# Performance work log

Measured on AMD Instinct MI355X. Metric: run time of the kernel, lower is better.

Reference implementation:

```python
import jax, jax.numpy as jnp
import numpy as np
from math import factorial

# ---- configuration (from init_kwargs irreps strings) ----
IRR1 = [(128, 0, 1), (128, 1, -1), (128, 2, 1)]   # (mul, l, parity)
IRR2 = [(1, 0, 1), (1, 1, -1), (1, 2, 1)]
IRRO = [(128, 0, 1), (128, 1, -1), (128, 2, 1)]
BATCH = 32768

# ---- real-basis Wigner 3j (e3nn convention: unit Frobenius norm) ----

def _cg_coeff(j1, m1, j2, m2, j3, m3):
    f = factorial
    vmin = int(max(-j1 + j2 + m3, -j1 + m1, 0))
    vmax = int(min(j2 + j3 + m1, j3 - j1 + j2, j3 + m3))
    C = ((2 * j3 + 1) * f(j3 + j1 - j2) * f(j3 - j1 + j2) * f(j1 + j2 - j3)
         * f(j3 + m3) * f(j3 - m3)
         / (f(j1 + j2 + j3 + 1) * f(j1 - m1) * f(j1 + m1) * f(j2 - m2) * f(j2 + m2))) ** 0.5
    S = 0.0
    for v in range(vmin, vmax + 1):
        S += (-1.0) ** (v + j2 + m2) * f(j2 + j3 + m1 - v) * f(j1 - m1 + v) / (
            f(v) * f(j3 - j1 + j2 - v) * f(j3 + m3 - v) * f(v + j1 - j2 - m3))
    return C * S


def _su2_cg(j1, j2, j3):
    m = np.zeros((2 * j1 + 1, 2 * j2 + 1, 2 * j3 + 1))
    for m1 in range(-j1, j1 + 1):
        for m2 in range(-j2, j2 + 1):
            m3 = m1 + m2
            if abs(m3) <= j3:
                m[j1 + m1, j2 + m2, j3 + m3] = _cg_coeff(j1, m1, j2, m2, j3, m3)
    return m


def _q(l):  # change of basis real -> complex spherical harmonics
    q = np.zeros((2 * l + 1, 2 * l + 1), dtype=np.complex128)
    for m in range(-l, 0):
        q[l + m, l + abs(m)] = 1 / np.sqrt(2)
        q[l + m, l - abs(m)] = -1j / np.sqrt(2)
    q[l, l] = 1.0
    for m in range(1, l + 1):
        q[l + m, l + abs(m)] = (-1) ** m / np.sqrt(2)
        q[l + m, l - abs(m)] = 1j * (-1) ** m / np.sqrt(2)
    return (-1j) ** l * q


def wigner_3j(l1, l2, l3):
    C = _su2_cg(l1, l2, l3).astype(np.complex128)
    C = np.einsum('ij,kl,mn,ikn->jlm', _q(l1), _q(l2), np.conj(_q(l3).T), C)
    C = np.real(C)
    return (C / np.linalg.norm(C)).astype(np.float32)


# ---- instructions: all allowed uvw paths (same triple loop as the torch module) ----

def _build_instructions():
    instr = []
    for i1, (m1, l1, p1) in enumerate(IRR1):
        for i2, (m2, l2, p2) in enumerate(IRR2):
            for io, (mo, lo, po) in enumerate(IRRO):
                if abs(l1 - l2) <= lo <= l1 + l2 and p1 * p2 == po:
                    instr.append((i1, i2, io))
    # e3nn defaults: irrep_normalization='component', path_normalization='element'
    elem = {}
    for (i1, i2, io) in instr:
        elem[io] = elem.get(io, 0) + IRR1[i1][0] * IRR2[i2][0]
    pathw = [((2 * IRRO[io][1] + 1) / elem[io]) ** 0.5 for (i1, i2, io) in instr]
    return instr, pathw

INSTR, PATHW = _build_instructions()
OFF1 = np.cumsum([0] + [m * (2 * l + 1) for m, l, _ in IRR1]).tolist()
OFF2 = np.cumsum([0] + [m * (2 * l + 1) for m, l, _ in IRR2]).tolist()
OFFO = np.cumsum([0] + [m * (2 * l + 1) for m, l, _ in IRRO]).tolist()
W3J = {(i1, i2, io): jnp.asarray(wigner_3j(IRR1[i1][1], IRR2[i2][1], IRRO[io][1]))
       for (i1, i2, io) in INSTR}


def setup_inputs() -> dict:
    key = jax.random.key(0)
    k1, k2, k3, k4 = jax.random.split(key, 4)
    n = len(INSTR)  # 11
    return {
        'x1': jax.random.normal(k1, (BATCH, OFF1[-1]), jnp.float32),
        'x2': jax.random.normal(k2, (BATCH, OFF2[-1]), jnp.float32),
        'w1': jax.random.normal(k3, (n, IRR1[0][0], IRRO[0][0]), jnp.float32),
        'w2': jax.random.normal(k4, (n, IRR2[0][0], IRRO[0][0]), jnp.float32),
    }


def reference(x1, x2, w1, w2):
    # fused per-path CG contraction: weight W[u,v,w] = w1[u,w] * w2[v,w]
    B = x1.shape[0]
    acc = [None] * len(IRRO)
    for idx, (i1, i2, io) in enumerate(INSTR):
        m1, l1, _ = IRR1[i1]
        m2, l2, _ = IRR2[i2]
        mo, lo, _ = IRRO[io]
        a = x1[:, OFF1[i1]:OFF1[i1 + 1]].reshape(B, m1, 2 * l1 + 1)  # (B,u,i)
        b = x2[:, OFF2[i2]:OFF2[i2 + 1]].reshape(B, m2, 2 * l2 + 1)  # (B,v,j)
        C = W3J[(i1, i2, io)] * PATHW[idx]                            # (i,j,k)
        o = jnp.einsum('uw,vw,ijk,bui,bvj->bwk', w1[idx], w2[idx], C, a, b,
                       optimize='optimal').reshape(B, mo * (2 * lo + 1))
        acc[io] = o if acc[io] is None else acc[io] + o
    return jnp.concatenate(acc, axis=1)
```

## Files before the change

kernel.cpp:

```cpp
#include <hip/hip_runtime.h>

typedef float f32x4v __attribute__((ext_vector_type(4)));
typedef short s16x8  __attribute__((ext_vector_type(8)));

#define MT 32

constexpr int cI1[11]   = {0,0,0,1,1,1,1,2,2,2,2};
constexpr int cI2[11]   = {0,1,2,0,1,1,2,0,1,2,2};
constexpr int cIO[11]   = {0,1,2,1,0,2,1,2,1,0,2};
constexpr int cSOFF[11] = {0,1,4,9,18,21,36,45,70,85,90};
constexpr int cOFF1[3]  = {0,128,512};
constexpr int cOFF2[3]  = {0,1,4};

__device__ __forceinline__ unsigned short f2bf(float f){
  unsigned int u = __float_as_uint(f);
  u = u + 0x7fffu + ((u>>16)&1u);
  return (unsigned short)(u>>16);
}

__device__ __forceinline__ float ffact(int n){ float r=1.f; for(int i=2;i<=n;++i) r*=(float)i; return r; }

__device__ float cg1f(int j1,int m1,int j2,int m2,int j3,int m3){
  int vmin = -j1+j2+m3; int t=-j1+m1; if(t>vmin)vmin=t; if(vmin<0)vmin=0;
  int vmax = j2+j3+m1; t=j3-j1+j2; if(t<vmax)vmax=t; t=j3+m3; if(t<vmax)vmax=t;
  float C = sqrtf((2.f*j3+1.f)*ffact(j3+j1-j2)*ffact(j3-j1+j2)*ffact(j1+j2-j3)
                 *ffact(j3+m3)*ffact(j3-m3)
                 /(ffact(j1+j2+j3+1)*ffact(j1-m1)*ffact(j1+m1)*ffact(j2-m2)*ffact(j2+m2)));
  float S=0.f;
  for(int v=vmin;v<=vmax;++v){
    float sg = ((v+j2+m2)&1)? -1.f:1.f;
    S += sg*ffact(j2+j3+m1-v)*ffact(j1-m1+v)
        /(ffact(v)*ffact(j3-j1+j2-v)*ffact(j3+m3-v)*ffact(v+j1-j2-m3));
  }
  return C*S;
}

__global__ void prep_cg(float* __restrict__ wsC){
  __shared__ float s_cg[125];
  __shared__ float s_qr[3][25], s_qi[3][25];
  __shared__ float s_out[125];
  __shared__ float s_inv;
  const int idx = blockIdx.x;
  const int l1=cI1[idx], l2=cI2[idx], l3=cIO[idx];
  const int n1=2*l1+1, n2=2*l2+1, n3=2*l3+1;
  const int tid = threadIdx.x;
  if (tid < 125) s_cg[tid] = 0.f;
  __syncthreads();
  if (tid < 75){
    const int mat=tid/25, e=tid%25, a=e/5, b=e%5;
    const int l = (mat==0)?l1:((mat==1)?l2:l3);
    const int n = 2*l+1;
    float r=0.f, im=0.f;
    if (a<n && b<n){
      const int m = a - l;
      const float s2 = 0.70710678118654752440f;
      if (m < 0){
        if (b == l-m) r = s2;
        else if (b == a) im = -s2;
      } else if (m == 0){
        if (b == a) r = 1.f;
      } else {
        const float sg = (m&1)? -1.f:1.f;
        if (b == a) r = sg*s2;
        else if (b == l-m) im = sg*s2;
      }
      const int ph = l & 3;
      if (ph == 1){ float t=r; r=im; im=-t; }
      else if (ph == 2){ r=-r; im=-im; }
      else if (ph == 3){ float t=r; r=-im; im=t; }
    }
    s_qr[mat][e] = r; s_qi[mat][e] = im;
  }
  if (tid < n1*n2){
    const int m1 = tid / n2 - l1;
    const int m2 = tid % n2 - l2;
    const int m3 = m1 + m2;
    if (m3 >= -l3 && m3 <= l3)
      s_cg[(l1+m1)*25 + (l2+m2)*5 + (l3+m3)] = cg1f(l1,m1,l2,m2,l3,m3);
  }
  __syncthreads();
  const int nElem = n1*n2*n3;
  if (tid < nElem){
    const int j = tid/(n2*n3);
    const int L = (tid/n3) % n2;
    const int m = tid % n3;
    float acc = 0.f;
    for (int i=0;i<n1;i++){
      const float ar=s_qr[0][i*5+j], ai=s_qi[0][i*5+j];
      for (int k=0;k<n2;k++){
        const float br=s_qr[1][k*5+L], bi=s_qi[1][k*5+L];
        const float pr=ar*br-ai*bi, pi=ar*bi+ai*br;
        for (int n=0;n<n3;n++){
          const float c=s_cg[i*25+k*5+n];
          acc += c*(pr*s_qr[2][n*5+m] + pi*s_qi[2][n*5+m]);
        }
      }
    }
    s_out[tid] = acc;
  }
  __syncthreads();
  if (tid == 0){
    float nrm = 0.f;
    for (int t=0;t<nElem;t++) nrm += s_out[t]*s_out[t];
    s_inv = rsqrtf(nrm);
  }
  __syncthreads();
  if (tid < 125){
    const int j=tid/25, L=(tid/5)%5, m=tid%5;
    float v = 0.f;
    if (j<n1 && L<n2 && m<n3) v = s_out[(j*n2+L)*n3+m] * s_inv;
    wsC[idx*125 + tid] = v;
  }
}

__global__ void prep_w(const float* __restrict__ w1, const float* __restrict__ w2,
                       unsigned char* __restrict__ wsB){
  int gid = blockIdx.x*256 + threadIdx.x;
  if (gid >= 11*8*4*64) return;
  int lane = gid & 63;
  int g = gid >> 6;
  int kst = g & 3, nt = (g>>2)&7, idx = g>>5;
  int io = cIO[idx];
  float pw = (io==0)?0.051031036307982884f:((io==1)?0.07654655446197431f:0.09882117688026186f);
  int u0 = kst*32 + ((lane>>4)&3)*8;
  int w  = nt*16 + (lane&15);
  float w2v = w2[idx*128 + w] * pw;
  s16x8 p;
  #pragma unroll
  for (int e=0;e<8;e++){
    float v = w1[idx*16384 + (u0+e)*128 + w] * w2v;
    p[e] = (short)f2bf(v);
  }
  *(s16x8*)(wsB + (size_t)g*1024 + (size_t)lane*16) = p;
}

template<int IDX, int NK>
__device__ __forceinline__ void do_idx(f32x4v (&acc)[NK][2],
    const float* __restrict__ x1, const unsigned char* __restrict__ wsB,
    unsigned char* lds, const float* s_lds, int brow0, int tid){
  constexpr int I1 = cI1[IDX];
  constexpr int NI = 2*I1+1;
  const int lane = tid & 63, wave = tid >> 6;
  const int mtile = wave >> 2, ng0 = (wave & 3)*2;
  s16x8 bfr[2][4];
  #pragma unroll
  for(int nt=0;nt<2;nt++)
    #pragma unroll
    for(int kst=0;kst<4;kst++)
      bfr[nt][kst] = *(const s16x8*)(wsB + (size_t)(((IDX*8 + ng0+nt)*4 + kst)*64 + lane)*16);
  const int tb = tid >> 4, tu0 = (tid & 15)*8;
  const float* xrow = x1 + (size_t)(brow0+tb)*1152 + cOFF1[I1] + tu0*NI;
  const int row = mtile*16 + (lane&15);
  const int rsw = (row&7)<<4;
  const int hi  = (lane>>4)&3;
  f32x4v xv[2*NI];
  #pragma unroll
  for(int f=0;f<2*NI;f++) xv[f] = ((const f32x4v*)xrow)[f];
  #pragma unroll
  for(int kc0=0;kc0<NK;kc0+=3){
    __syncthreads();
    #pragma unroll
    for(int kk=0;kk<3;kk++) if(kc0+kk<NK){
      const int k=kc0+kk;
      float sv[NI];
      #pragma unroll
      for(int i=0;i<NI;i++) sv[i]=s_lds[tb*116 + cSOFF[IDX] + i*NK + k];
      s16x8 tp;
      #pragma unroll
      for(int u=0;u<8;u++){
        float tvv=0.0f;
        #pragma unroll
        for(int i=0;i<NI;i++){ const int n=u*NI+i; tvv += sv[i]*xv[n>>2][n&3]; }
        tp[u]=(short)f2bf(tvv);
      }
      *(s16x8*)(lds + kk*8192 + tb*256 + ((tu0*2) ^ ((tb&7)<<4))) = tp;
    }
    __syncthreads();
    #pragma unroll
    for(int kk=0;kk<3;kk++) if(kc0+kk<NK){
      #pragma unroll
      for(int kst=0;kst<4;kst++){
        s16x8 af = *(const s16x8*)(lds + kk*8192 + row*256 + ((kst*64 + hi*16) ^ rsw));
        #pragma unroll
        for(int nt=0;nt<2;nt++)
          acc[kc0+kk][nt] = __builtin_amdgcn_mfma_f32_16x16x32_bf16(af, bfr[nt][kst], acc[kc0+kk][nt], 0,0,0);
      }
    }
  }
}

template<int OO, int NK>
__device__ __forceinline__ void store_group(f32x4v (&acc)[NK][2], float* __restrict__ out, int brow0, int tid){
  const int lane=tid&63, wave=tid>>6;
  const int mtile=wave>>2, ng0=(wave&3)*2;
  const int r0 = brow0 + mtile*16 + ((lane>>4)&3)*4;
  #pragma unroll
  for(int nt=0;nt<2;nt++){
    const int w = (ng0+nt)*16 + (lane&15);
    #pragma unroll
    for(int k=0;k<NK;k++){
      #pragma unroll
      for(int rr=0;rr<4;rr++)
        out[(size_t)(r0+rr)*1152 + OO + w*NK + k] = acc[k][nt][rr];
    }
  }
}

__global__ __launch_bounds__(512) void tp_main(
    const float* __restrict__ x1, const float* __restrict__ x2,
    const float* __restrict__ wsC, const unsigned char* __restrict__ wsB,
    float* __restrict__ out){
  __shared__ __attribute__((aligned(16))) unsigned char lds[24576 + 32*116*4];
  float* s_lds = (float*)(lds + 24576);
  const int tid = threadIdx.x;
  const int brow0 = blockIdx.x * MT;
  if (tid < 352){
    const int b = tid & 31, idx = tid >> 5;
    const int i1=cI1[idx], i2=cI2[idx], io=cIO[idx];
    const int ni=2*i1+1, nj=2*i2+1, nk=2*io+1;
    const float* x2r = x2 + (size_t)(brow0+b)*9 + cOFF2[i2];
    const float* C = wsC + idx*125;
    float xv[5];
    for(int j=0;j<nj;j++) xv[j]=x2r[j];
    for(int i=0;i<ni;i++)
      for(int k=0;k<nk;k++){
        float s=0.f;
        for(int j=0;j<nj;j++) s += C[i*25+j*5+k]*xv[j];
        s_lds[b*116 + cSOFF[idx] + i*nk + k] = s;
      }
  }
  {
    f32x4v acc[1][2] = {};
    do_idx<0,1>(acc,x1,wsB,lds,s_lds,brow0,tid);
    do_idx<4,1>(acc,x1,wsB,lds,s_lds,brow0,tid);
    do_idx<9,1>(acc,x1,wsB,lds,s_lds,brow0,tid);
    store_group<0,1>(acc,out,brow0,tid);
  }
  {
    f32x4v acc[3][2] = {};
    do_idx<1,3>(acc,x1,wsB,lds,s_lds,brow0,tid);
    do_idx<3,3>(acc,x1,wsB,lds,s_lds,brow0,tid);
    do_idx<6,3>(acc,x1,wsB,lds,s_lds,brow0,tid);
    do_idx<8,3>(acc,x1,wsB,lds,s_lds,brow0,tid);
    store_group<128,3>(acc,out,brow0,tid);
  }
  {
    f32x4v acc[5][2] = {};
    do_idx<2,5>(acc,x1,wsB,lds,s_lds,brow0,tid);
    do_idx<5,5>(acc,x1,wsB,lds,s_lds,brow0,tid);
    do_idx<7,5>(acc,x1,wsB,lds,s_lds,brow0,tid);
    do_idx<10,5>(acc,x1,wsB,lds,s_lds,brow0,tid);
    store_group<512,5>(acc,out,brow0,tid);
  }
}

extern "C" void kernel_launch(void* const* d_in, const int* in_sizes, int n_in,
                              void* d_out, int out_size, void* d_ws, size_t ws_size,
                              hipStream_t stream) {
  const float* x1 = (const float*)d_in[0];
  const float* x2 = (const float*)d_in[1];
  const float* w1 = (const float*)d_in[2];
  const float* w2 = (const float*)d_in[3];
  float* out = (float*)d_out;
  float* wsC = (float*)d_ws;
  unsigned char* wsB = (unsigned char*)d_ws + 8192;
  prep_cg<<<11, 128, 0, stream>>>(wsC);
  prep_w<<<88, 256, 0, stream>>>(w1, w2, wsB);
  tp_main<<<32768/MT, 512, 0, stream>>>(x1, x2, wsC, wsB, out);
}
```

Baseline: 408.9 us.

## Double-buffer LDS tiles and software-pipeline T build with MFMA consumption

Replaces the per-path loop (sync, build bf16 T tile in LDS, sync, MFMA) with a hand-unrolled software pipeline over two LDS buffers. The build of the next chunk and the prefetch of the next x1 rows and B fragments overlap the MFMAs on the current buffer, and one barrier per stage replaces two. LDS use doubles to about 61 KB per block, which may reduce how many blocks fit per CU, and register pressure rises from the prefetched xv and bfr.

```diff
diff --git a/kernel.cpp b/kernel.cpp
--- a/kernel.cpp
+++ b/kernel.cpp
@@ -134,57 +134,63 @@
   *(s16x8*)(wsB + (size_t)g*1024 + (size_t)lane*16) = p;
 }
 
-template<int IDX, int NK>
-__device__ __forceinline__ void do_idx(f32x4v (&acc)[NK][2],
-    const float* __restrict__ x1, const unsigned char* __restrict__ wsB,
-    unsigned char* lds, const float* s_lds, int brow0, int tid){
-  constexpr int I1 = cI1[IDX];
-  constexpr int NI = 2*I1+1;
-  const int lane = tid & 63, wave = tid >> 6;
-  const int mtile = wave >> 2, ng0 = (wave & 3)*2;
-  s16x8 bfr[2][4];
+
+template<int IDX>
+__device__ __forceinline__ void xv_load(f32x4v (&xv)[10], const float* __restrict__ x1, int brow0, int tid){
+  constexpr int NI = 2*cI1[IDX]+1;
+  const int tb = tid>>4, tu0 = (tid&15)*8;
+  const float* xrow = x1 + (size_t)(brow0+tb)*1152 + cOFF1[cI1[IDX]] + tu0*NI;
+  #pragma unroll
+  for(int f=0; f<2*NI; f++) xv[f] = ((const f32x4v*)xrow)[f];
+}
+
+template<int IDX>
+__device__ __forceinline__ void bfr_load(s16x8 (&bfr)[2][4], const unsigned char* __restrict__ wsB, int tid){
+  const int lane=tid&63, wave=tid>>6, ng0=(wave&3)*2;
   #pragma unroll
   for(int nt=0;nt<2;nt++)
     #pragma unroll
     for(int kst=0;kst<4;kst++)
-      bfr[nt][kst] = *(const s16x8*)(wsB + (size_t)(((IDX*8 + ng0+nt)*4 + kst)*64 + lane)*16);
-  const int tb = tid >> 4, tu0 = (tid & 15)*8;
-  const float* xrow = x1 + (size_t)(brow0+tb)*1152 + cOFF1[I1] + tu0*NI;
+      bfr[nt][kst] = *(const s16x8*)(wsB + (size_t)(((IDX*8+ng0+nt)*4+kst)*64+lane)*16);
+}
+
+template<int IDX, int NK, int KB, int NKC>
+__device__ __forceinline__ void t_build(const f32x4v (&xv)[10], unsigned char* buf,
+                                        const float* s_lds, int tid){
+  constexpr int NI = 2*cI1[IDX]+1;
+  const int tb = tid>>4, tu0=(tid&15)*8;
+  #pragma unroll
+  for(int kk=0;kk<NKC;kk++){
+    const int k = KB+kk;
+    float sv[NI];
+    #pragma unroll
+    for(int i=0;i<NI;i++) sv[i] = s_lds[tb*116 + cSOFF[IDX] + i*NK + k];
+    s16x8 tp;
+    #pragma unroll
+    for(int u=0;u<8;u++){
+      float t=0.f;
+      #pragma unroll
+      for(int i=0;i<NI;i++){ const int n=u*NI+i; t += sv[i]*xv[n>>2][n&3]; }
+      tp[u]=(short)f2bf(t);
+    }
+    *(s16x8*)(buf + kk*8192 + tb*256 + ((tu0*2) ^ ((tb&7)<<4))) = tp;
+  }
+}
+
+template<int NACC, int KB, int NKC>
+__device__ __forceinline__ void mfma_cons(f32x4v (&acc)[NACC][2], const s16x8 (&bfr)[2][4],
+                                          const unsigned char* buf, int tid){
+  const int lane=tid&63, wave=tid>>6, mtile=wave>>2;
   const int row = mtile*16 + (lane&15);
-  const int rsw = (row&7)<<4;
-  const int hi  = (lane>>4)&3;
-  f32x4v xv[2*NI];
-  #pragma unroll
-  for(int f=0;f<2*NI;f++) xv[f] = ((const f32x4v*)xrow)[f];
-  #pragma unroll
-  for(int kc0=0;kc0<NK;kc0+=3){
-    __syncthreads();
-    #pragma unroll
-    for(int kk=0;kk<3;kk++) if(kc0+kk<NK){
-      const int k=kc0+kk;
-      float sv[NI];
+  const int rsw = (row&7)<<4, hi=(lane>>4)&3;
+  #pragma unroll
+  for(int kk=0;kk<NKC;kk++){
+    #pragma unroll
+    for(int kst=0;kst<4;kst++){
+      s16x8 af = *(const s16x8*)(buf + kk*8192 + row*256 + ((kst*64+hi*16)^rsw));
       #pragma unroll
-      for(int i=0;i<NI;i++) sv[i]=s_lds[tb*116 + cSOFF[IDX] + i*NK + k];
-      s16x8 tp;
-      #pragma unroll
-      for(int u=0;u<8;u++){
-        float tvv=0.0f;
-        #pragma unroll
-        for(int i=0;i<NI;i++){ const int n=u*NI+i; tvv += sv[i]*xv[n>>2][n&3]; }
-        tp[u]=(short)f2bf(tvv);
-      }
-      *(s16x8*)(lds + kk*8192 + tb*256 + ((tu0*2) ^ ((tb&7)<<4))) = tp;
-    }
-    __syncthreads();
-    #pragma unroll
-    for(int kk=0;kk<3;kk++) if(kc0+kk<NK){
-      #pragma unroll
-      for(int kst=0;kst<4;kst++){
-        s16x8 af = *(const s16x8*)(lds + kk*8192 + row*256 + ((kst*64 + hi*16) ^ rsw));
-        #pragma unroll
-        for(int nt=0;nt<2;nt++)
-          acc[kc0+kk][nt] = __builtin_amdgcn_mfma_f32_16x16x32_bf16(af, bfr[nt][kst], acc[kc0+kk][nt], 0,0,0);
-      }
+      for(int nt=0;nt<2;nt++)
+        acc[KB+kk][nt] = __builtin_amdgcn_mfma_f32_16x16x32_bf16(af, bfr[nt][kst], acc[KB+kk][nt],0,0,0);
     }
   }
 }
@@ -210,47 +216,112 @@
     const float* __restrict__ x1, const float* __restrict__ x2,
     const float* __restrict__ wsC, const unsigned char* __restrict__ wsB,
     float* __restrict__ out){
-  __shared__ __attribute__((aligned(16))) unsigned char lds[24576 + 32*116*4];
-  float* s_lds = (float*)(lds + 24576);
+  __shared__ __attribute__((aligned(16))) unsigned char lds[49152 + 32*116*4];
+  unsigned char* buf0 = lds;
+  unsigned char* buf1 = lds + 24576;
+  float* s_lds = (float*)(lds + 49152);
   const int tid = threadIdx.x;
   const int brow0 = blockIdx.x * MT;
+
   if (tid < 352){
     const int b = tid & 31, idx = tid >> 5;
     const int i1=cI1[idx], i2=cI2[idx], io=cIO[idx];
     const int ni=2*i1+1, nj=2*i2+1, nk=2*io+1;
     const float* x2r = x2 + (size_t)(brow0+b)*9 + cOFF2[i2];
     const float* C = wsC + idx*125;
-    float xv[5];
-    for(int j=0;j<nj;j++) xv[j]=x2r[j];
+    float xv2[5];
+    for(int j=0;j<nj;j++) xv2[j]=x2r[j];
     for(int i=0;i<ni;i++)
       for(int k=0;k<nk;k++){
         float s=0.f;
-        for(int j=0;j<nj;j++) s += C[i*25+j*5+k]*xv[j];
+        for(int j=0;j<nj;j++) s += C[i*25+j*5+k]*xv2[j];
         s_lds[b*116 + cSOFF[idx] + i*nk + k] = s;
       }
   }
+
+  f32x4v xv[10];
+  s16x8 bfr[2][4];
+
+  xv_load<0>(xv, x1, brow0, tid);
+  bfr_load<0>(bfr, wsB, tid);
+  __syncthreads();
+  t_build<0,1,0,1>(xv, buf0, s_lds, tid);
+  xv_load<4>(xv, x1, brow0, tid);
+  __syncthreads();
+
   {
-    f32x4v acc[1][2] = {};
-    do_idx<0,1>(acc,x1,wsB,lds,s_lds,brow0,tid);
-    do_idx<4,1>(acc,x1,wsB,lds,s_lds,brow0,tid);
-    do_idx<9,1>(acc,x1,wsB,lds,s_lds,brow0,tid);
-    store_group<0,1>(acc,out,brow0,tid);
+    f32x4v accA[1][2] = {};
+    mfma_cons<1,0,1>(accA, bfr, buf0, tid);
+    t_build<4,1,0,1>(xv, buf1, s_lds, tid);
+    xv_load<9>(xv, x1, brow0, tid);
+    bfr_load<4>(bfr, wsB, tid);
+    __syncthreads();
+    mfma_cons<1,0,1>(accA, bfr, buf1, tid);
+    t_build<9,1,0,1>(xv, buf0, s_lds, tid);
+    xv_load<1>(xv, x1, brow0, tid);
+    bfr_load<9>(bfr, wsB, tid);
+    __syncthreads();
+    mfma_cons<1,0,1>(accA, bfr, buf0, tid);
+    t_build<1,3,0,3>(xv, buf1, s_lds, tid);
+    xv_load<3>(xv, x1, brow0, tid);
+    bfr_load<1>(bfr, wsB, tid);
+    store_group<0,1>(accA, out, brow0, tid);
+    __syncthreads();
   }
   {
-    f32x4v acc[3][2] = {};
-    do_idx<1,3>(acc,x1,wsB,lds,s_lds,brow0,tid);
-    do_idx<3,3>(acc,x1,wsB,lds,s_lds,brow0,tid);
-    do_idx<6,3>(acc,x1,wsB,lds,s_lds,brow0,tid);
-    do_idx<8,3>(acc,x1,wsB,lds,s_lds,brow0,tid);
-    store_group<128,3>(acc,out,brow0,tid);
+    f32x4v accB[3][2] = {};
+    mfma_cons<3,0,3>(accB, bfr, buf1, tid);
+    t_build<3,3,0,3>(xv, buf0, s_lds, tid);
+    xv_load<6>(xv, x1, brow0, tid);
+    bfr_load<3>(bfr, wsB, tid);
+    __syncthreads();
+    mfma_cons<3,0,3>(accB, bfr, buf0, tid);
+    t_build<6,3,0,3>(xv, buf1, s_lds, tid);
+    xv_load<8>(xv, x1, brow0, tid);
+    bfr_load<6>(bfr, wsB, tid);
+    __syncthreads();
+    mfma_cons<3,0,3>(accB, bfr, buf1, tid);
+    t_build<8,3,0,3>(xv, buf0, s_lds, tid);
+    xv_load<2>(xv, x1, brow0, tid);
+    bfr_load<8>(bfr, wsB, tid);
+    __syncthreads();
+    mfma_cons<3,0,3>(accB, bfr, buf0, tid);
+    t_build<2,5,0,3>(xv, buf1, s_lds, tid);
+    bfr_load<2>(bfr, wsB, tid);
+    store_group<128,3>(accB, out, brow0, tid);
+    __syncthreads();
   }
   {
-    f32x4v acc[5][2] = {};
-    do_idx<2,5>(acc,x1,wsB,lds,s_lds,brow0,tid);
-    do_idx<5,5>(acc,x1,wsB,lds,s_lds,brow0,tid);
-    do_idx<7,5>(acc,x1,wsB,lds,s_lds,brow0,tid);
-    do_idx<10,5>(acc,x1,wsB,lds,s_lds,brow0,tid);
-    store_group<512,5>(acc,out,brow0,tid);
+    f32x4v accC[5][2] = {};
+    mfma_cons<5,0,3>(accC, bfr, buf1, tid);
+    t_build<2,5,3,2>(xv, buf0, s_lds, tid);
+    xv_load<5>(xv, x1, brow0, tid);
+    __syncthreads();
+    mfma_cons<5,3,2>(accC, bfr, buf0, tid);
+    t_build<5,5,0,3>(xv, buf1, s_lds, tid);
+    bfr_load<5>(bfr, wsB, tid);
+    __syncthreads();
+    mfma_cons<5,0,3>(accC, bfr, buf1, tid);
+    t_build<5,5,3,2>(xv, buf0, s_lds, tid);
+    xv_load<7>(xv, x1, brow0, tid);
+    __syncthreads();
+    mfma_cons<5,3,2>(accC, bfr, buf0, tid);
+    t_build<7,5,0,3>(xv, buf1, s_lds, tid);
+    bfr_load<7>(bfr, wsB, tid);
+    __syncthreads();
+    mfma_cons<5,0,3>(accC, bfr, buf1, tid);
+    t_build<7,5,3,2>(xv, buf0, s_lds, tid);
+    xv_load<10>(xv, x1, brow0, tid);
+    __syncthreads();
+    mfma_cons<5,3,2>(accC, bfr, buf0, tid);
+    t_build<10,5,0,3>(xv, buf1, s_lds, tid);
+    bfr_load<10>(bfr, wsB, tid);
+    __syncthreads();
+    mfma_cons<5,0,3>(accC, bfr, buf1, tid);
+    t_build<10,5,3,2>(xv, buf0, s_lds, tid);
+    __syncthreads();
+    mfma_cons<5,3,2>(accC, bfr, buf0, tid);
+    store_group<512,5>(accC, out, brow0, tid);
   }
 }
 
```

Measured after the change: 389.7 us. -4.7%, faster.

## Reorder contraction to GEMM per x1 component, then scale by CG-x2 terms

Applied to the files above, without the earlier changes.

Each x1 irrep block is now converted to bf16 and staged in LDS once, split by component. The kernel then runs one MFMA GEMM per component i, then applies the per-row s[b,i,k] coefficients to the fp32 results and adds them into accumulators held for all three outputs. Before, it built a separate combined activation tile for every (path, k) pair. This cuts the repeated x1 global loads, the fp32 combine work, the bf16 conversions and the barriers per path. In exchange, all three accumulator sets stay live at once, which raises register pressure, and the staging step uses strided scalar global reads.

```diff
diff --git a/kernel.cpp b/kernel.cpp
--- a/kernel.cpp
+++ b/kernel.cpp
@@ -134,56 +134,78 @@
   *(s16x8*)(wsB + (size_t)g*1024 + (size_t)lane*16) = p;
 }
 
-template<int IDX, int NK>
-__device__ __forceinline__ void do_idx(f32x4v (&acc)[NK][2],
-    const float* __restrict__ x1, const unsigned char* __restrict__ wsB,
-    unsigned char* lds, const float* s_lds, int brow0, int tid){
-  constexpr int I1 = cI1[IDX];
+
+template<int I1>
+__device__ __forceinline__ void stage_x(const float* __restrict__ x1, unsigned char* xt,
+                                        int brow0, int tid){
   constexpr int NI = 2*I1+1;
-  const int lane = tid & 63, wave = tid >> 6;
-  const int mtile = wave >> 2, ng0 = (wave & 3)*2;
+  const int b = tid>>4, oct = tid&15;
+  const float* src = x1 + (size_t)(brow0+b)*1152 + cOFF1[I1];
+  const int dsw = (oct*16) ^ ((b&7)<<4);
+  if constexpr (I1==0){
+    f32x4v v0 = *(const f32x4v*)(src + oct*8);
+    f32x4v v1 = *(const f32x4v*)(src + oct*8 + 4);
+    s16x8 p;
+    #pragma unroll
+    for(int e=0;e<4;e++){ p[e]=(short)f2bf(v0[e]); p[4+e]=(short)f2bf(v1[e]); }
+    *(s16x8*)(xt + b*256 + dsw) = p;
+  } else if constexpr (I1==1){
+    s16x8 p0, p1, p2;
+    #pragma unroll
+    for(int e=0;e<8;e++){
+      const float* q = src + (oct*8+e)*3;
+      p0[e]=(short)f2bf(q[0]); p1[e]=(short)f2bf(q[1]); p2[e]=(short)f2bf(q[2]);
+    }
+    *(s16x8*)(xt            + b*256 + dsw) = p0;
+    *(s16x8*)(xt +   8192   + b*256 + dsw) = p1;
+    *(s16x8*)(xt + 2*8192   + b*256 + dsw) = p2;
+  } else {
+    s16x8 p0, p1, p2, p3, p4;
+    #pragma unroll
+    for(int e=0;e<8;e++){
+      const float* q = src + (oct*8+e)*5;
+      p0[e]=(short)f2bf(q[0]); p1[e]=(short)f2bf(q[1]); p2[e]=(short)f2bf(q[2]);
+      p3[e]=(short)f2bf(q[3]); p4[e]=(short)f2bf(q[4]);
+    }
+    *(s16x8*)(xt            + b*256 + dsw) = p0;
+    *(s16x8*)(xt +   8192   + b*256 + dsw) = p1;
+    *(s16x8*)(xt + 2*8192   + b*256 + dsw) = p2;
+    *(s16x8*)(xt + 3*8192   + b*256 + dsw) = p3;
+    *(s16x8*)(xt + 4*8192   + b*256 + dsw) = p4;
+  }
+}
+
+template<int P, int NKT>
+__device__ __forceinline__ void path_compute(f32x4v (&acc)[NKT][2],
+    const unsigned char* xt, const float* s_lds, const unsigned char* __restrict__ wsB, int tid){
+  constexpr int NI = 2*cI1[P]+1;
+  const int lane=tid&63, wave=tid>>6, mtile=wave>>2, ng0=(wave&3)*2;
   s16x8 bfr[2][4];
   #pragma unroll
   for(int nt=0;nt<2;nt++)
     #pragma unroll
     for(int kst=0;kst<4;kst++)
-      bfr[nt][kst] = *(const s16x8*)(wsB + (size_t)(((IDX*8 + ng0+nt)*4 + kst)*64 + lane)*16);
-  const int tb = tid >> 4, tu0 = (tid & 15)*8;
-  const float* xrow = x1 + (size_t)(brow0+tb)*1152 + cOFF1[I1] + tu0*NI;
-  const int row = mtile*16 + (lane&15);
-  const int rsw = (row&7)<<4;
-  const int hi  = (lane>>4)&3;
-  f32x4v xv[2*NI];
-  #pragma unroll
-  for(int f=0;f<2*NI;f++) xv[f] = ((const f32x4v*)xrow)[f];
-  #pragma unroll
-  for(int kc0=0;kc0<NK;kc0+=3){
-    __syncthreads();
-    #pragma unroll
-    for(int kk=0;kk<3;kk++) if(kc0+kk<NK){
-      const int k=kc0+kk;
-      float sv[NI];
+      bfr[nt][kst] = *(const s16x8*)(wsB + (size_t)(((P*8+ng0+nt)*4+kst)*64+lane)*16);
+  const int arow = mtile*16 + (lane&15);
+  const int rsw  = (arow&7)<<4;
+  const int hi   = lane>>4;
+  const int sbase = (mtile*16 + hi*4)*116 + cSOFF[P];
+  #pragma unroll
+  for(int i=0;i<NI;i++){
+    f32x4v Y0 = {0.f,0.f,0.f,0.f}, Y1 = {0.f,0.f,0.f,0.f};
+    #pragma unroll
+    for(int kst=0;kst<4;kst++){
+      s16x8 af = *(const s16x8*)(xt + i*8192 + arow*256 + ((kst*64 + hi*16) ^ rsw));
+      Y0 = __builtin_amdgcn_mfma_f32_16x16x32_bf16(af, bfr[0][kst], Y0, 0,0,0);
+      Y1 = __builtin_amdgcn_mfma_f32_16x16x32_bf16(af, bfr[1][kst], Y1, 0,0,0);
+    }
+    #pragma unroll
+    for(int r=0;r<4;r++){
       #pragma unroll
-      for(int i=0;i<NI;i++) sv[i]=s_lds[tb*116 + cSOFF[IDX] + i*NK + k];
-      s16x8 tp;
-      #pragma unroll
-      for(int u=0;u<8;u++){
-        float tvv=0.0f;
-        #pragma unroll
-        for(int i=0;i<NI;i++){ const int n=u*NI+i; tvv += sv[i]*xv[n>>2][n&3]; }
-        tp[u]=(short)f2bf(tvv);
-      }
-      *(s16x8*)(lds + kk*8192 + tb*256 + ((tu0*2) ^ ((tb&7)<<4))) = tp;
-    }
-    __syncthreads();
-    #pragma unroll
-    for(int kk=0;kk<3;kk++) if(kc0+kk<NK){
-      #pragma unroll
-      for(int kst=0;kst<4;kst++){
-        s16x8 af = *(const s16x8*)(lds + kk*8192 + row*256 + ((kst*64 + hi*16) ^ rsw));
-        #pragma unroll
-        for(int nt=0;nt<2;nt++)
-          acc[kc0+kk][nt] = __builtin_amdgcn_mfma_f32_16x16x32_bf16(af, bfr[nt][kst], acc[kc0+kk][nt], 0,0,0);
+      for(int k=0;k<NKT;k++){
+        const float sv = s_lds[sbase + r*116 + i*NKT + k];
+        acc[k][0][r] += sv * Y0[r];
+        acc[k][1][r] += sv * Y1[r];
       }
     }
   }
@@ -210,48 +232,55 @@
     const float* __restrict__ x1, const float* __restrict__ x2,
     const float* __restrict__ wsC, const unsigned char* __restrict__ wsB,
     float* __restrict__ out){
-  __shared__ __attribute__((aligned(16))) unsigned char lds[24576 + 32*116*4];
-  float* s_lds = (float*)(lds + 24576);
+  __shared__ __attribute__((aligned(16))) unsigned char lds[40960 + 32*116*4];
+  unsigned char* xt = lds;
+  float* s_lds = (float*)(lds + 40960);
   const int tid = threadIdx.x;
   const int brow0 = blockIdx.x * MT;
+
   if (tid < 352){
     const int b = tid & 31, idx = tid >> 5;
     const int i1=cI1[idx], i2=cI2[idx], io=cIO[idx];
     const int ni=2*i1+1, nj=2*i2+1, nk=2*io+1;
     const float* x2r = x2 + (size_t)(brow0+b)*9 + cOFF2[i2];
     const float* C = wsC + idx*125;
-    float xv[5];
-    for(int j=0;j<nj;j++) xv[j]=x2r[j];
+    float xv2[5];
+    for(int j=0;j<nj;j++) xv2[j]=x2r[j];
     for(int i=0;i<ni;i++)
       for(int k=0;k<nk;k++){
         float s=0.f;
-        for(int j=0;j<nj;j++) s += C[i*25+j*5+k]*xv[j];
+        for(int j=0;j<nj;j++) s += C[i*25+j*5+k]*xv2[j];
         s_lds[b*116 + cSOFF[idx] + i*nk + k] = s;
       }
   }
-  {
-    f32x4v acc[1][2] = {};
-    do_idx<0,1>(acc,x1,wsB,lds,s_lds,brow0,tid);
-    do_idx<4,1>(acc,x1,wsB,lds,s_lds,brow0,tid);
-    do_idx<9,1>(acc,x1,wsB,lds,s_lds,brow0,tid);
-    store_group<0,1>(acc,out,brow0,tid);
-  }
-  {
-    f32x4v acc[3][2] = {};
-    do_idx<1,3>(acc,x1,wsB,lds,s_lds,brow0,tid);
-    do_idx<3,3>(acc,x1,wsB,lds,s_lds,brow0,tid);
-    do_idx<6,3>(acc,x1,wsB,lds,s_lds,brow0,tid);
-    do_idx<8,3>(acc,x1,wsB,lds,s_lds,brow0,tid);
-    store_group<128,3>(acc,out,brow0,tid);
-  }
-  {
-    f32x4v acc[5][2] = {};
-    do_idx<2,5>(acc,x1,wsB,lds,s_lds,brow0,tid);
-    do_idx<5,5>(acc,x1,wsB,lds,s_lds,brow0,tid);
-    do_idx<7,5>(acc,x1,wsB,lds,s_lds,brow0,tid);
-    do_idx<10,5>(acc,x1,wsB,lds,s_lds,brow0,tid);
-    store_group<512,5>(acc,out,brow0,tid);
-  }
+  stage_x<0>(x1, xt, brow0, tid);
+
+  f32x4v accA[1][2] = {};
+  f32x4v accB[3][2] = {};
+  f32x4v accC[5][2] = {};
+
+  __syncthreads();
+  path_compute<0,1>(accA, xt, s_lds, wsB, tid);
+  path_compute<1,3>(accB, xt, s_lds, wsB, tid);
+  path_compute<2,5>(accC, xt, s_lds, wsB, tid);
+  __syncthreads();
+  stage_x<1>(x1, xt, brow0, tid);
+  __syncthreads();
+  path_compute<3,3>(accB, xt, s_lds, wsB, tid);
+  path_compute<4,1>(accA, xt, s_lds, wsB, tid);
+  path_compute<5,5>(accC, xt, s_lds, wsB, tid);
+  path_compute<6,3>(accB, xt, s_lds, wsB, tid);
+  __syncthreads();
+  stage_x<2>(x1, xt, brow0, tid);
+  __syncthreads();
+  path_compute<7,5>(accC, xt, s_lds, wsB, tid);
+  path_compute<8,3>(accB, xt, s_lds, wsB, tid);
+  path_compute<9,1>(accA, xt, s_lds, wsB, tid);
+  path_compute<10,5>(accC, xt, s_lds, wsB, tid);
+
+  store_group<0,1>(accA, out, brow0, tid);
+  store_group<128,3>(accB, out, brow0, tid);
+  store_group<512,5>(accC, out, brow0, tid);
 }
 
 extern "C" void kernel_launch(void* const* d_in, const int* in_sizes, int n_in,
```

Measured after the change: 751.3 us. +83.8%, slower.
